# Performance work log

Measured on AMD Instinct MI355X. Metric: run time of the kernel, lower is better.

The kernel has to match this reference:

```python
import jax, jax.numpy as jnp
import numpy as np

T, B, I, H, L = 256, 128, 512, 1024, 4

def setup_inputs() -> dict:
    key = jax.random.key(0)
    ks = jax.random.split(key, 8)
    s = 1.0 / np.sqrt(H)  # ~PyTorch GRU init scale U(-1/sqrt(H), 1/sqrt(H))
    x = jax.random.normal(ks[0], (T, B, I), dtype=jnp.float32)
    hidden = jnp.zeros((L, B, H), dtype=jnp.float32)  # initHidden
    w_ih0 = jax.random.normal(ks[1], (3 * H, I), dtype=jnp.float32) * s
    w_ih_rest = jax.random.normal(ks[2], (L - 1, 3 * H, H), dtype=jnp.float32) * s
    w_hh = jax.random.normal(ks[3], (L, 3 * H, H), dtype=jnp.float32) * s
    b_ih = jax.random.normal(ks[4], (L, 3 * H), dtype=jnp.float32) * s
    b_hh = jax.random.normal(ks[5], (L, 3 * H), dtype=jnp.float32) * s
    input_lengths = jax.random.randint(ks[6], (B,), 1, T + 1)
    return {"x": x, "hidden": hidden, "w_ih0": w_ih0, "w_ih_rest": w_ih_rest,
            "w_hh": w_hh, "b_ih": b_ih, "b_hh": b_hh,
            "total_length": T, "input_lengths": input_lengths}

def _gru_layer(xs, h0, w_ih, w_hh_l, bi, bh, mask):
    # xs: (T,B,D_in); h0: (B,H); mask: (T,B) bool (t < length)
    gi = jnp.einsum('tbd,gd->tbg', xs, w_ih) + bi  # (T,B,3H) input GEMM hoisted out of scan
    def step(h, inp):
        gi_t, m = inp  # (B,3H), (B,)
        gh = h @ w_hh_l.T + bh  # (B,3H)
        ir, iz, inn = jnp.split(gi_t, 3, axis=-1)  # PyTorch gate order: r, z, n
        hr, hz, hn = jnp.split(gh, 3, axis=-1)
        r = jax.nn.sigmoid(ir + hr)
        z = jax.nn.sigmoid(iz + hz)
        n = jnp.tanh(inn + r * hn)
        h_new = (1.0 - z) * n + z * h
        m2 = m[:, None]
        h_next = jnp.where(m2, h_new, h)            # packed-seq: state frozen past length
        y = jnp.where(m2, h_new, jnp.zeros_like(h))  # pad_packed_sequence zero-pads output
        return h_next, y
    hT, ys = jax.lax.scan(step, h0, (gi, mask))
    return ys, hT

def reference(x, hidden, w_ih0, w_ih_rest, w_hh, b_ih, b_hh, total_length, input_lengths):
    # dropout=0.2 between layers is disabled (deterministic / eval mode)
    mask = jnp.arange(total_length)[:, None] < input_lengths[None, :]  # (T,B)
    ys = x
    h_finals = []
    for l in range(L):
        w_ih_l = w_ih0 if l == 0 else w_ih_rest[l - 1]
        ys, hT = _gru_layer(ys, hidden[l], w_ih_l, w_hh[l], b_ih[l], b_hh[l], mask)
        h_finals.append(hT)
    return ys, jnp.stack(h_finals, axis=0)  # (T,B,H), (4,B,H)
```

## Files before the change

kernel.cpp:

```cpp
#include <hip/hip_runtime.h>
#include <hip/hip_bf16.h>

#define T_STEPS 256
#define BATCH   128
#define IDIM    512
#define HDIM    1024
#define NLAYERS 4
#define G3      (3 * HDIM)
#define BH      (BATCH * HDIM)

typedef __bf16 bf16_t;
typedef __bf16 bf16x4 __attribute__((ext_vector_type(4)));
typedef __bf16 bf16x8 __attribute__((ext_vector_type(8)));
typedef float  f32x4  __attribute__((ext_vector_type(4)));

__device__ __forceinline__ float sigm_f(float x) { return 1.0f / (1.0f + __expf(-x)); }
__device__ __forceinline__ float tanh_f(float x) { return 1.0f - 2.0f / (__expf(2.0f * x) + 1.0f); }

__device__ __forceinline__ bf16x8 cvt8(const float* p) {
    f32x4 v0 = *(const f32x4*)p;
    f32x4 v1 = *(const f32x4*)(p + 4);
    bf16x8 o;
    o[0] = (bf16_t)v0[0]; o[1] = (bf16_t)v0[1]; o[2] = (bf16_t)v0[2]; o[3] = (bf16_t)v0[3];
    o[4] = (bf16_t)v1[0]; o[5] = (bf16_t)v1[1]; o[6] = (bf16_t)v1[2]; o[7] = (bf16_t)v1[3];
    return o;
}

__global__ void cvt_f2b(const float* __restrict__ s, bf16_t* __restrict__ d, int n4) {
    int i = blockIdx.x * blockDim.x + threadIdx.x;
    if (i < n4) {
        f32x4 v = ((const f32x4*)s)[i];
        bf16x4 o;
        o[0] = (bf16_t)v[0]; o[1] = (bf16_t)v[1];
        o[2] = (bf16_t)v[2]; o[3] = (bf16_t)v[3];
        ((bf16x4*)d)[i] = o;
    }
}

__global__ void split_h(const float* __restrict__ s,
                        bf16_t* __restrict__ hi, bf16_t* __restrict__ lo) {
    int i = blockIdx.x * blockDim.x + threadIdx.x;
    f32x4 v = ((const f32x4*)s)[i];
    bf16x4 h, l;
#pragma unroll
    for (int j = 0; j < 4; ++j) {
        bf16_t t = (bf16_t)v[j];
        h[j] = t;
        l[j] = (bf16_t)(v[j] - (float)t);
    }
    ((bf16x4*)hi)[i] = h;
    ((bf16x4*)lo)[i] = l;
}

template <int HIN>
__global__ __launch_bounds__(64)
void gi_gemm(const float*  __restrict__ ysrc,
             const bf16_t* __restrict__ w_ih,
             const float*  __restrict__ b_ih,
             float* __restrict__ gi,
             int row0)
{
    const int lane = threadIdx.x;
    const int cq   = lane & 15;
    const int quad = lane >> 4;
    const int n0   = blockIdx.x * 64;
    const int m0   = blockIdx.y * 32;

    const float* a0p = ysrc + (size_t)(row0 + m0 + cq) * HIN + quad * 8;
    const float* a1p = a0p + (size_t)16 * HIN;
    const bf16_t* b0p = w_ih + (size_t)(n0 + cq) * HIN + quad * 8;
    const bf16_t* b1p = b0p + (size_t)16 * HIN;
    const bf16_t* b2p = b0p + (size_t)32 * HIN;
    const bf16_t* b3p = b0p + (size_t)48 * HIN;

    f32x4 a00{0,0,0,0}, a01 = a00, a02 = a00, a03 = a00;
    f32x4 a10 = a00, a11 = a00, a12 = a00, a13 = a00;

#pragma unroll 4
    for (int k = 0; k < HIN; k += 32) {
        bf16x8 fa0 = cvt8(a0p + k);
        bf16x8 fa1 = cvt8(a1p + k);
        bf16x8 fb0 = *(const bf16x8*)(b0p + k);
        bf16x8 fb1 = *(const bf16x8*)(b1p + k);
        bf16x8 fb2 = *(const bf16x8*)(b2p + k);
        bf16x8 fb3 = *(const bf16x8*)(b3p + k);
        a00 = __builtin_amdgcn_mfma_f32_16x16x32_bf16(fa0, fb0, a00, 0, 0, 0);
        a01 = __builtin_amdgcn_mfma_f32_16x16x32_bf16(fa0, fb1, a01, 0, 0, 0);
        a02 = __builtin_amdgcn_mfma_f32_16x16x32_bf16(fa0, fb2, a02, 0, 0, 0);
        a03 = __builtin_amdgcn_mfma_f32_16x16x32_bf16(fa0, fb3, a03, 0, 0, 0);
        a10 = __builtin_amdgcn_mfma_f32_16x16x32_bf16(fa1, fb0, a10, 0, 0, 0);
        a11 = __builtin_amdgcn_mfma_f32_16x16x32_bf16(fa1, fb1, a11, 0, 0, 0);
        a12 = __builtin_amdgcn_mfma_f32_16x16x32_bf16(fa1, fb2, a12, 0, 0, 0);
        a13 = __builtin_amdgcn_mfma_f32_16x16x32_bf16(fa1, fb3, a13, 0, 0, 0);
    }

    const float bb0 = b_ih[n0 + 0  + cq];
    const float bb1 = b_ih[n0 + 16 + cq];
    const float bb2 = b_ih[n0 + 32 + cq];
    const float bb3 = b_ih[n0 + 48 + cq];

#pragma unroll
    for (int i = 0; i < 4; ++i) {
        const int r0 = m0 + quad * 4 + i;
        const int r1 = r0 + 16;
        float* g0 = gi + (size_t)r0 * G3 + n0 + cq;
        float* g1 = gi + (size_t)r1 * G3 + n0 + cq;
        g0[0]  = a00[i] + bb0;  g0[16] = a01[i] + bb1;
        g0[32] = a02[i] + bb2;  g0[48] = a03[i] + bb3;
        g1[0]  = a10[i] + bb0;  g1[16] = a11[i] + bb1;
        g1[32] = a12[i] + bb2;  g1[48] = a13[i] + bb3;
    }
}

struct LayerStep {
    const float*  gi_t;
    const bf16_t* w_hh;
    const float*  b_hh;
    const bf16_t* h_in_hi;
    const bf16_t* h_in_lo;
    bf16_t*       h_out_hi;
    bf16_t*       h_out_lo;
    float*        y_t;
    float*        h_final;
    int           t;
};
struct StepArgs { LayerStep L[NLAYERS]; };

__global__ __launch_bounds__(512)
void gru_step_multi(StepArgs args, const int* __restrict__ lengths)
{
    __shared__ f32x4 red[4][3][2][2][2][64];

    const LayerStep& A = args.L[blockIdx.z];

    const int tid  = threadIdx.x;
    const int wid  = tid >> 6;
    const int lane = tid & 63;
    const int cq   = lane & 15;
    const int quad = lane >> 4;
    const int c0   = blockIdx.x * 32;
    const int m0   = blockIdx.y * 64;

    const int kq = wid & 3;
    const int rh = wid >> 2;
    const int kofs = kq * 256 + quad * 8;

    const bf16_t* aph0 = A.h_in_hi + (size_t)(m0 + rh * 32 + cq) * HDIM + kofs;
    const bf16_t* aph1 = aph0 + (size_t)16 * HDIM;
    const bf16_t* apl0 = A.h_in_lo + (size_t)(m0 + rh * 32 + cq) * HDIM + kofs;
    const bf16_t* apl1 = apl0 + (size_t)16 * HDIM;
    const bf16_t* bp00 = A.w_hh + (size_t)(0 * HDIM + c0 + cq) * HDIM + kofs;
    const bf16_t* bp01 = bp00 + (size_t)16 * HDIM;
    const bf16_t* bp10 = A.w_hh + (size_t)(1 * HDIM + c0 + cq) * HDIM + kofs;
    const bf16_t* bp11 = bp10 + (size_t)16 * HDIM;
    const bf16_t* bp20 = A.w_hh + (size_t)(2 * HDIM + c0 + cq) * HDIM + kofs;
    const bf16_t* bp21 = bp20 + (size_t)16 * HDIM;

    f32x4 acc[2][2][3];
#pragma unroll
    for (int rf = 0; rf < 2; ++rf)
#pragma unroll
        for (int cf = 0; cf < 2; ++cf)
#pragma unroll
            for (int g = 0; g < 3; ++g) acc[rf][cf][g] = f32x4{0, 0, 0, 0};

#pragma unroll
    for (int k = 0; k < 256; k += 32) {
        bf16x8 Ah[2], Al[2], Bv[3][2];
        Ah[0] = *(const bf16x8*)(aph0 + k);
        Ah[1] = *(const bf16x8*)(aph1 + k);
        Al[0] = *(const bf16x8*)(apl0 + k);
        Al[1] = *(const bf16x8*)(apl1 + k);
        Bv[0][0] = *(const bf16x8*)(bp00 + k);
        Bv[0][1] = *(const bf16x8*)(bp01 + k);
        Bv[1][0] = *(const bf16x8*)(bp10 + k);
        Bv[1][1] = *(const bf16x8*)(bp11 + k);
        Bv[2][0] = *(const bf16x8*)(bp20 + k);
        Bv[2][1] = *(const bf16x8*)(bp21 + k);
#pragma unroll
        for (int rf = 0; rf < 2; ++rf)
#pragma unroll
            for (int cf = 0; cf < 2; ++cf)
#pragma unroll
                for (int g = 0; g < 3; ++g)
                    acc[rf][cf][g] = __builtin_amdgcn_mfma_f32_16x16x32_bf16(
                        Ah[rf], Bv[g][cf], acc[rf][cf][g], 0, 0, 0);
#pragma unroll
        for (int rf = 0; rf < 2; ++rf)
#pragma unroll
            for (int cf = 0; cf < 2; ++cf)
#pragma unroll
                for (int g = 0; g < 3; ++g)
                    acc[rf][cf][g] = __builtin_amdgcn_mfma_f32_16x16x32_bf16(
                        Al[rf], Bv[g][cf], acc[rf][cf][g], 0, 0, 0);
    }

#pragma unroll
    for (int rf = 0; rf < 2; ++rf)
#pragma unroll
        for (int cf = 0; cf < 2; ++cf)
#pragma unroll
            for (int g = 0; g < 3; ++g)
                red[kq][g][rh][rf][cf][lane] = acc[rf][cf][g];
    __syncthreads();

    {
        const int grh = wid & 1;
        const int grf = (wid >> 1) & 1;
        const int gcf = wid >> 2;
        const int col = c0 + gcf * 16 + cq;

        f32x4 sr = ((red[0][0][grh][grf][gcf][lane] + red[1][0][grh][grf][gcf][lane])
                  +  red[2][0][grh][grf][gcf][lane]) + red[3][0][grh][grf][gcf][lane];
        f32x4 sz = ((red[0][1][grh][grf][gcf][lane] + red[1][1][grh][grf][gcf][lane])
                  +  red[2][1][grh][grf][gcf][lane]) + red[3][1][grh][grf][gcf][lane];
        f32x4 sn = ((red[0][2][grh][grf][gcf][lane] + red[1][2][grh][grf][gcf][lane])
                  +  red[2][2][grh][grf][gcf][lane]) + red[3][2][grh][grf][gcf][lane];

        const float bhr = A.b_hh[col];
        const float bhz = A.b_hh[HDIM + col];
        const float bhn = A.b_hh[2 * HDIM + col];

#pragma unroll
        for (int i = 0; i < 4; ++i) {
            const int row = m0 + grh * 32 + grf * 16 + quad * 4 + i;
            const size_t oh = (size_t)row * HDIM + col;
            const float* gr = A.gi_t + (size_t)row * G3;
            const float ir  = gr[col];
            const float iz  = gr[HDIM + col];
            const float inn = gr[2 * HDIM + col];
            const float hold = (float)A.h_in_hi[oh] + (float)A.h_in_lo[oh];
            const float r = sigm_f(ir + sr[i] + bhr);
            const float z = sigm_f(iz + sz[i] + bhz);
            const float n = tanh_f(inn + r * (sn[i] + bhn));
            const float hnew = (1.0f - z) * n + z * hold;
            const bool msk = A.t < lengths[row];
            const float hnext = msk ? hnew : hold;
            const bf16_t hb = (bf16_t)hnext;
            A.h_out_hi[oh] = hb;
            A.h_out_lo[oh] = (bf16_t)(hnext - (float)hb);
            A.y_t[oh] = msk ? hnew : 0.0f;
            if (A.h_final) A.h_final[oh] = hnext;
        }
    }
}

extern "C" void kernel_launch(void* const* d_in, const int* in_sizes, int n_in,
                              void* d_out, int out_size, void* d_ws, size_t ws_size,
                              hipStream_t stream) {
    const float* x         = (const float*)d_in[0];
    const float* hidden    = (const float*)d_in[1];
    const float* w_ih0     = (const float*)d_in[2];
    const float* w_ih_rest = (const float*)d_in[3];
    const float* w_hh      = (const float*)d_in[4];
    const float* b_ih      = (const float*)d_in[5];
    const float* b_hh      = (const float*)d_in[6];
    const int*   lengths   = (const int*)d_in[8];

    float* ys   = (float*)d_out;
    float* hfin = ys + (size_t)T_STEPS * BH;

    char* ws = (char*)d_ws;
    bf16_t* wb_ih0  = (bf16_t*)ws;
    bf16_t* wb_rest = wb_ih0 + (size_t)G3 * IDIM;
    bf16_t* wb_hh   = wb_rest + (size_t)(NLAYERS - 1) * G3 * HDIM;
    bf16_t* hbase   = wb_hh + (size_t)NLAYERS * G3 * HDIM;
    float*  gi_base = (float*)(hbase + (size_t)NLAYERS * 4 * BH);

    const size_t fixed_bytes = (size_t)((char*)gi_base - ws);
    int chunk = 16;
    while (chunk > 2 &&
           fixed_bytes + (size_t)NLAYERS * chunk * BATCH * G3 * sizeof(float) > ws_size)
        chunk >>= 1;
    const int nch = T_STEPS / chunk;
    const size_t gi_stride = (size_t)chunk * BATCH * G3;

    {
        int n4;
        n4 = G3 * IDIM / 4;
        cvt_f2b<<<(n4 + 255) / 256, 256, 0, stream>>>(w_ih0, wb_ih0, n4);
        n4 = (NLAYERS - 1) * G3 * HDIM / 4;
        cvt_f2b<<<(n4 + 255) / 256, 256, 0, stream>>>(w_ih_rest, wb_rest, n4);
        n4 = NLAYERS * G3 * HDIM / 4;
        cvt_f2b<<<(n4 + 255) / 256, 256, 0, stream>>>(w_hh, wb_hh, n4);
    }

    for (int l = 0; l < NLAYERS; ++l) {
        bf16_t* hb = hbase + (size_t)l * 4 * BH;
        split_h<<<BH / 4 / 256, 256, 0, stream>>>(hidden + (size_t)l * BH, hb, hb + BH);
    }

    const dim3 gridA(G3 / 64, chunk * BATCH / 32);

    for (int s = 0; s < nch + NLAYERS - 1; ++s) {
        for (int l = 0; l < NLAYERS; ++l) {
            const int c = s - l;
            if (c < 0 || c >= nch) continue;
            float* gi_l = gi_base + (size_t)l * gi_stride;
            const bf16_t* wb_ih_l = (l == 0) ? wb_ih0 : (wb_rest + (size_t)(l - 1) * G3 * HDIM);
            const float*  b_ih_l  = b_ih + (size_t)l * G3;
            const int row0 = c * chunk * BATCH;
            if (l == 0) {
                gi_gemm<IDIM><<<gridA, 64, 0, stream>>>(x, wb_ih_l, b_ih_l, gi_l, row0);
            } else {
                gi_gemm<HDIM><<<gridA, 64, 0, stream>>>(ys, wb_ih_l, b_ih_l, gi_l, row0);
            }
        }
        for (int tt = 0; tt < chunk; ++tt) {
            StepArgs sa;
            int na = 0;
            for (int l = 0; l < NLAYERS; ++l) {
                const int c = s - l;
                if (c < 0 || c >= nch) continue;
                const int t = c * chunk + tt;
                const bool rd0 = ((t & 1) == 0);
                bf16_t* hb = hbase + (size_t)l * 4 * BH;
                bf16_t* hhi0 = hb, *hlo0 = hb + BH, *hhi1 = hb + 2 * BH, *hlo1 = hb + 3 * BH;
                LayerStep& P = sa.L[na++];
                P.gi_t     = gi_base + (size_t)l * gi_stride + (size_t)tt * BATCH * G3;
                P.w_hh     = wb_hh + (size_t)l * G3 * HDIM;
                P.b_hh     = b_hh + (size_t)l * G3;
                P.h_in_hi  = rd0 ? hhi0 : hhi1;
                P.h_in_lo  = rd0 ? hlo0 : hlo1;
                P.h_out_hi = rd0 ? hhi1 : hhi0;
                P.h_out_lo = rd0 ? hlo1 : hlo0;
                P.y_t      = ys + (size_t)t * BH;
                P.h_final  = (t == T_STEPS - 1) ? (hfin + (size_t)l * BH) : nullptr;
                P.t        = t;
            }
            dim3 gridB(HDIM / 32, BATCH / 64, na);
            gru_step_multi<<<gridB, 512, 0, stream>>>(sa, lengths);
        }
    }
}
```

Baseline: 12.14 ms.

## Fuse input-gate GEMM into per-step GRU kernel with bf16 ring buffers

Removes the separate chunked gi_gemm launches and computes the input projection inside the recurrent step kernel, accumulating r/z gates from both input and hidden contributions in shared accumulators. Inter-layer activations are kept as bf16 in a per-layer ring buffer, and x is pre-converted to bf16, so the fp32 gi scratch traffic and kernel launches disappear. The trade-off is more MFMA work and weight bandwidth on the serial critical path of every step, since the input GEMM no longer runs as a large batched GEMM. The ring of 2*CHUNK slots relies on the wavefront layer schedule to avoid overwriting activations that have not yet been consumed.

```diff
diff --git a/kernel.cpp b/kernel.cpp
--- a/kernel.cpp
+++ b/kernel.cpp
@@ -8,6 +8,8 @@
 #define NLAYERS 4
 #define G3      (3 * HDIM)
 #define BH      (BATCH * HDIM)
+#define CHUNK   16
+#define RING    (2 * CHUNK)
 
 typedef __bf16 bf16_t;
 typedef __bf16 bf16x4 __attribute__((ext_vector_type(4)));
@@ -16,15 +18,6 @@
 
 __device__ __forceinline__ float sigm_f(float x) { return 1.0f / (1.0f + __expf(-x)); }
 __device__ __forceinline__ float tanh_f(float x) { return 1.0f - 2.0f / (__expf(2.0f * x) + 1.0f); }
-
-__device__ __forceinline__ bf16x8 cvt8(const float* p) {
-    f32x4 v0 = *(const f32x4*)p;
-    f32x4 v1 = *(const f32x4*)(p + 4);
-    bf16x8 o;
-    o[0] = (bf16_t)v0[0]; o[1] = (bf16_t)v0[1]; o[2] = (bf16_t)v0[2]; o[3] = (bf16_t)v0[3];
-    o[4] = (bf16_t)v1[0]; o[5] = (bf16_t)v1[1]; o[6] = (bf16_t)v1[2]; o[7] = (bf16_t)v1[3];
-    return o;
-}
 
 __global__ void cvt_f2b(const float* __restrict__ s, bf16_t* __restrict__ d, int n4) {
     int i = blockIdx.x * blockDim.x + threadIdx.x;
@@ -52,84 +45,28 @@
     ((bf16x4*)lo)[i] = l;
 }
 
-template <int HIN>
-__global__ __launch_bounds__(64)
-void gi_gemm(const float*  __restrict__ ysrc,
-             const bf16_t* __restrict__ w_ih,
-             const float*  __restrict__ b_ih,
-             float* __restrict__ gi,
-             int row0)
-{
-    const int lane = threadIdx.x;
-    const int cq   = lane & 15;
-    const int quad = lane >> 4;
-    const int n0   = blockIdx.x * 64;
-    const int m0   = blockIdx.y * 32;
-
-    const float* a0p = ysrc + (size_t)(row0 + m0 + cq) * HIN + quad * 8;
-    const float* a1p = a0p + (size_t)16 * HIN;
-    const bf16_t* b0p = w_ih + (size_t)(n0 + cq) * HIN + quad * 8;
-    const bf16_t* b1p = b0p + (size_t)16 * HIN;
-    const bf16_t* b2p = b0p + (size_t)32 * HIN;
-    const bf16_t* b3p = b0p + (size_t)48 * HIN;
-
-    f32x4 a00{0,0,0,0}, a01 = a00, a02 = a00, a03 = a00;
-    f32x4 a10 = a00, a11 = a00, a12 = a00, a13 = a00;
-
-#pragma unroll 4
-    for (int k = 0; k < HIN; k += 32) {
-        bf16x8 fa0 = cvt8(a0p + k);
-        bf16x8 fa1 = cvt8(a1p + k);
-        bf16x8 fb0 = *(const bf16x8*)(b0p + k);
-        bf16x8 fb1 = *(const bf16x8*)(b1p + k);
-        bf16x8 fb2 = *(const bf16x8*)(b2p + k);
-        bf16x8 fb3 = *(const bf16x8*)(b3p + k);
-        a00 = __builtin_amdgcn_mfma_f32_16x16x32_bf16(fa0, fb0, a00, 0, 0, 0);
-        a01 = __builtin_amdgcn_mfma_f32_16x16x32_bf16(fa0, fb1, a01, 0, 0, 0);
-        a02 = __builtin_amdgcn_mfma_f32_16x16x32_bf16(fa0, fb2, a02, 0, 0, 0);
-        a03 = __builtin_amdgcn_mfma_f32_16x16x32_bf16(fa0, fb3, a03, 0, 0, 0);
-        a10 = __builtin_amdgcn_mfma_f32_16x16x32_bf16(fa1, fb0, a10, 0, 0, 0);
-        a11 = __builtin_amdgcn_mfma_f32_16x16x32_bf16(fa1, fb1, a11, 0, 0, 0);
-        a12 = __builtin_amdgcn_mfma_f32_16x16x32_bf16(fa1, fb2, a12, 0, 0, 0);
-        a13 = __builtin_amdgcn_mfma_f32_16x16x32_bf16(fa1, fb3, a13, 0, 0, 0);
-    }
-
-    const float bb0 = b_ih[n0 + 0  + cq];
-    const float bb1 = b_ih[n0 + 16 + cq];
-    const float bb2 = b_ih[n0 + 32 + cq];
-    const float bb3 = b_ih[n0 + 48 + cq];
-
-#pragma unroll
-    for (int i = 0; i < 4; ++i) {
-        const int r0 = m0 + quad * 4 + i;
-        const int r1 = r0 + 16;
-        float* g0 = gi + (size_t)r0 * G3 + n0 + cq;
-        float* g1 = gi + (size_t)r1 * G3 + n0 + cq;
-        g0[0]  = a00[i] + bb0;  g0[16] = a01[i] + bb1;
-        g0[32] = a02[i] + bb2;  g0[48] = a03[i] + bb3;
-        g1[0]  = a10[i] + bb0;  g1[16] = a11[i] + bb1;
-        g1[32] = a12[i] + bb2;  g1[48] = a13[i] + bb3;
-    }
-}
-
 struct LayerStep {
-    const float*  gi_t;
+    const bf16_t* inp;
+    const bf16_t* w_ih;
     const bf16_t* w_hh;
+    const float*  b_ih;
     const float*  b_hh;
     const bf16_t* h_in_hi;
     const bf16_t* h_in_lo;
     bf16_t*       h_out_hi;
     bf16_t*       h_out_lo;
-    float*        y_t;
+    bf16_t*       y_bf;
+    float*        y_f32;
     float*        h_final;
     int           t;
+    int           kin;
 };
 struct StepArgs { LayerStep L[NLAYERS]; };
 
 __global__ __launch_bounds__(512)
 void gru_step_multi(StepArgs args, const int* __restrict__ lengths)
 {
-    __shared__ f32x4 red[4][3][2][2][2][64];
+    __shared__ f32x4 red[4][4][2][2][2][64];
 
     const LayerStep& A = args.L[blockIdx.z];
 
@@ -143,65 +80,118 @@
 
     const int kq = wid & 3;
     const int rh = wid >> 2;
-    const int kofs = kq * 256 + quad * 8;
-
-    const bf16_t* aph0 = A.h_in_hi + (size_t)(m0 + rh * 32 + cq) * HDIM + kofs;
-    const bf16_t* aph1 = aph0 + (size_t)16 * HDIM;
-    const bf16_t* apl0 = A.h_in_lo + (size_t)(m0 + rh * 32 + cq) * HDIM + kofs;
-    const bf16_t* apl1 = apl0 + (size_t)16 * HDIM;
-    const bf16_t* bp00 = A.w_hh + (size_t)(0 * HDIM + c0 + cq) * HDIM + kofs;
-    const bf16_t* bp01 = bp00 + (size_t)16 * HDIM;
-    const bf16_t* bp10 = A.w_hh + (size_t)(1 * HDIM + c0 + cq) * HDIM + kofs;
-    const bf16_t* bp11 = bp10 + (size_t)16 * HDIM;
-    const bf16_t* bp20 = A.w_hh + (size_t)(2 * HDIM + c0 + cq) * HDIM + kofs;
-    const bf16_t* bp21 = bp20 + (size_t)16 * HDIM;
-
-    f32x4 acc[2][2][3];
+
+    f32x4 arz[2][2][2];
+    f32x4 ahn[2][2];
+    f32x4 ain[2][2];
 #pragma unroll
     for (int rf = 0; rf < 2; ++rf)
 #pragma unroll
-        for (int cf = 0; cf < 2; ++cf)
-#pragma unroll
-            for (int g = 0; g < 3; ++g) acc[rf][cf][g] = f32x4{0, 0, 0, 0};
-
-#pragma unroll
-    for (int k = 0; k < 256; k += 32) {
-        bf16x8 Ah[2], Al[2], Bv[3][2];
-        Ah[0] = *(const bf16x8*)(aph0 + k);
-        Ah[1] = *(const bf16x8*)(aph1 + k);
-        Al[0] = *(const bf16x8*)(apl0 + k);
-        Al[1] = *(const bf16x8*)(apl1 + k);
-        Bv[0][0] = *(const bf16x8*)(bp00 + k);
-        Bv[0][1] = *(const bf16x8*)(bp01 + k);
-        Bv[1][0] = *(const bf16x8*)(bp10 + k);
-        Bv[1][1] = *(const bf16x8*)(bp11 + k);
-        Bv[2][0] = *(const bf16x8*)(bp20 + k);
-        Bv[2][1] = *(const bf16x8*)(bp21 + k);
-#pragma unroll
-        for (int rf = 0; rf < 2; ++rf)
-#pragma unroll
-            for (int cf = 0; cf < 2; ++cf)
-#pragma unroll
-                for (int g = 0; g < 3; ++g)
-                    acc[rf][cf][g] = __builtin_amdgcn_mfma_f32_16x16x32_bf16(
-                        Ah[rf], Bv[g][cf], acc[rf][cf][g], 0, 0, 0);
-#pragma unroll
-        for (int rf = 0; rf < 2; ++rf)
-#pragma unroll
-            for (int cf = 0; cf < 2; ++cf)
-#pragma unroll
-                for (int g = 0; g < 3; ++g)
-                    acc[rf][cf][g] = __builtin_amdgcn_mfma_f32_16x16x32_bf16(
-                        Al[rf], Bv[g][cf], acc[rf][cf][g], 0, 0, 0);
+        for (int cf = 0; cf < 2; ++cf) {
+            arz[rf][cf][0] = f32x4{0, 0, 0, 0};
+            arz[rf][cf][1] = f32x4{0, 0, 0, 0};
+            ahn[rf][cf]    = f32x4{0, 0, 0, 0};
+            ain[rf][cf]    = f32x4{0, 0, 0, 0};
+        }
+
+    {
+        const int kofs = kq * 256 + quad * 8;
+        const bf16_t* aph0 = A.h_in_hi + (size_t)(m0 + rh * 32 + cq) * HDIM + kofs;
+        const bf16_t* aph1 = aph0 + (size_t)16 * HDIM;
+        const bf16_t* apl0 = A.h_in_lo + (size_t)(m0 + rh * 32 + cq) * HDIM + kofs;
+        const bf16_t* apl1 = apl0 + (size_t)16 * HDIM;
+        const bf16_t* bp00 = A.w_hh + (size_t)(0 * HDIM + c0 + cq) * HDIM + kofs;
+        const bf16_t* bp01 = bp00 + (size_t)16 * HDIM;
+        const bf16_t* bp10 = A.w_hh + (size_t)(1 * HDIM + c0 + cq) * HDIM + kofs;
+        const bf16_t* bp11 = bp10 + (size_t)16 * HDIM;
+        const bf16_t* bp20 = A.w_hh + (size_t)(2 * HDIM + c0 + cq) * HDIM + kofs;
+        const bf16_t* bp21 = bp20 + (size_t)16 * HDIM;
+
+#pragma unroll
+        for (int k = 0; k < 256; k += 32) {
+            bf16x8 Ah[2], Al[2], Bv[3][2];
+            Ah[0] = *(const bf16x8*)(aph0 + k);
+            Ah[1] = *(const bf16x8*)(aph1 + k);
+            Al[0] = *(const bf16x8*)(apl0 + k);
+            Al[1] = *(const bf16x8*)(apl1 + k);
+            Bv[0][0] = *(const bf16x8*)(bp00 + k);
+            Bv[0][1] = *(const bf16x8*)(bp01 + k);
+            Bv[1][0] = *(const bf16x8*)(bp10 + k);
+            Bv[1][1] = *(const bf16x8*)(bp11 + k);
+            Bv[2][0] = *(const bf16x8*)(bp20 + k);
+            Bv[2][1] = *(const bf16x8*)(bp21 + k);
+#pragma unroll
+            for (int rf = 0; rf < 2; ++rf)
+#pragma unroll
+                for (int cf = 0; cf < 2; ++cf) {
+                    arz[rf][cf][0] = __builtin_amdgcn_mfma_f32_16x16x32_bf16(
+                        Ah[rf], Bv[0][cf], arz[rf][cf][0], 0, 0, 0);
+                    arz[rf][cf][1] = __builtin_amdgcn_mfma_f32_16x16x32_bf16(
+                        Ah[rf], Bv[1][cf], arz[rf][cf][1], 0, 0, 0);
+                    ahn[rf][cf] = __builtin_amdgcn_mfma_f32_16x16x32_bf16(
+                        Ah[rf], Bv[2][cf], ahn[rf][cf], 0, 0, 0);
+                }
+#pragma unroll
+            for (int rf = 0; rf < 2; ++rf)
+#pragma unroll
+                for (int cf = 0; cf < 2; ++cf) {
+                    arz[rf][cf][0] = __builtin_amdgcn_mfma_f32_16x16x32_bf16(
+                        Al[rf], Bv[0][cf], arz[rf][cf][0], 0, 0, 0);
+                    arz[rf][cf][1] = __builtin_amdgcn_mfma_f32_16x16x32_bf16(
+                        Al[rf], Bv[1][cf], arz[rf][cf][1], 0, 0, 0);
+                    ahn[rf][cf] = __builtin_amdgcn_mfma_f32_16x16x32_bf16(
+                        Al[rf], Bv[2][cf], ahn[rf][cf], 0, 0, 0);
+                }
+        }
+    }
+
+    {
+        const int kin  = A.kin;
+        const int qw   = kin >> 2;
+        const int kofs = kq * qw + quad * 8;
+        const bf16_t* axp0 = A.inp + (size_t)(m0 + rh * 32 + cq) * kin + kofs;
+        const bf16_t* axp1 = axp0 + (size_t)16 * kin;
+        const bf16_t* wp00 = A.w_ih + (size_t)(0 * HDIM + c0 + cq) * kin + kofs;
+        const bf16_t* wp01 = wp00 + (size_t)16 * kin;
+        const bf16_t* wp10 = A.w_ih + (size_t)(1 * HDIM + c0 + cq) * kin + kofs;
+        const bf16_t* wp11 = wp10 + (size_t)16 * kin;
+        const bf16_t* wp20 = A.w_ih + (size_t)(2 * HDIM + c0 + cq) * kin + kofs;
+        const bf16_t* wp21 = wp20 + (size_t)16 * kin;
+
+#pragma unroll 4
+        for (int k = 0; k < qw; k += 32) {
+            bf16x8 Ax[2], Wv[3][2];
+            Ax[0] = *(const bf16x8*)(axp0 + k);
+            Ax[1] = *(const bf16x8*)(axp1 + k);
+            Wv[0][0] = *(const bf16x8*)(wp00 + k);
+            Wv[0][1] = *(const bf16x8*)(wp01 + k);
+            Wv[1][0] = *(const bf16x8*)(wp10 + k);
+            Wv[1][1] = *(const bf16x8*)(wp11 + k);
+            Wv[2][0] = *(const bf16x8*)(wp20 + k);
+            Wv[2][1] = *(const bf16x8*)(wp21 + k);
+#pragma unroll
+            for (int rf = 0; rf < 2; ++rf)
+#pragma unroll
+                for (int cf = 0; cf < 2; ++cf) {
+                    arz[rf][cf][0] = __builtin_amdgcn_mfma_f32_16x16x32_bf16(
+                        Ax[rf], Wv[0][cf], arz[rf][cf][0], 0, 0, 0);
+                    arz[rf][cf][1] = __builtin_amdgcn_mfma_f32_16x16x32_bf16(
+                        Ax[rf], Wv[1][cf], arz[rf][cf][1], 0, 0, 0);
+                    ain[rf][cf] = __builtin_amdgcn_mfma_f32_16x16x32_bf16(
+                        Ax[rf], Wv[2][cf], ain[rf][cf], 0, 0, 0);
+                }
+        }
     }
 
 #pragma unroll
     for (int rf = 0; rf < 2; ++rf)
 #pragma unroll
-        for (int cf = 0; cf < 2; ++cf)
-#pragma unroll
-            for (int g = 0; g < 3; ++g)
-                red[kq][g][rh][rf][cf][lane] = acc[rf][cf][g];
+        for (int cf = 0; cf < 2; ++cf) {
+            red[kq][0][rh][rf][cf][lane] = arz[rf][cf][0];
+            red[kq][1][rh][rf][cf][lane] = arz[rf][cf][1];
+            red[kq][2][rh][rf][cf][lane] = ahn[rf][cf];
+            red[kq][3][rh][rf][cf][lane] = ain[rf][cf];
+        }
     __syncthreads();
 
     {
@@ -214,9 +204,14 @@
                   +  red[2][0][grh][grf][gcf][lane]) + red[3][0][grh][grf][gcf][lane];
         f32x4 sz = ((red[0][1][grh][grf][gcf][lane] + red[1][1][grh][grf][gcf][lane])
                   +  red[2][1][grh][grf][gcf][lane]) + red[3][1][grh][grf][gcf][lane];
-        f32x4 sn = ((red[0][2][grh][grf][gcf][lane] + red[1][2][grh][grf][gcf][lane])
-                  +  red[2][2][grh][grf][gcf][lane]) + red[3][2][grh][grf][gcf][lane];
-
+        f32x4 shn = ((red[0][2][grh][grf][gcf][lane] + red[1][2][grh][grf][gcf][lane])
+                   +  red[2][2][grh][grf][gcf][lane]) + red[3][2][grh][grf][gcf][lane];
+        f32x4 sin_ = ((red[0][3][grh][grf][gcf][lane] + red[1][3][grh][grf][gcf][lane])
+                    +  red[2][3][grh][grf][gcf][lane]) + red[3][3][grh][grf][gcf][lane];
+
+        const float bir = A.b_ih[col];
+        const float biz = A.b_ih[HDIM + col];
+        const float bin = A.b_ih[2 * HDIM + col];
         const float bhr = A.b_hh[col];
         const float bhz = A.b_hh[HDIM + col];
         const float bhn = A.b_hh[2 * HDIM + col];
@@ -225,21 +220,19 @@
         for (int i = 0; i < 4; ++i) {
             const int row = m0 + grh * 32 + grf * 16 + quad * 4 + i;
             const size_t oh = (size_t)row * HDIM + col;
-            const float* gr = A.gi_t + (size_t)row * G3;
-            const float ir  = gr[col];
-            const float iz  = gr[HDIM + col];
-            const float inn = gr[2 * HDIM + col];
             const float hold = (float)A.h_in_hi[oh] + (float)A.h_in_lo[oh];
-            const float r = sigm_f(ir + sr[i] + bhr);
-            const float z = sigm_f(iz + sz[i] + bhz);
-            const float n = tanh_f(inn + r * (sn[i] + bhn));
+            const float r = sigm_f(sr[i] + bir + bhr);
+            const float z = sigm_f(sz[i] + biz + bhz);
+            const float n = tanh_f((sin_[i] + bin) + r * (shn[i] + bhn));
             const float hnew = (1.0f - z) * n + z * hold;
             const bool msk = A.t < lengths[row];
             const float hnext = msk ? hnew : hold;
             const bf16_t hb = (bf16_t)hnext;
             A.h_out_hi[oh] = hb;
             A.h_out_lo[oh] = (bf16_t)(hnext - (float)hb);
-            A.y_t[oh] = msk ? hnew : 0.0f;
+            const float yv = msk ? hnew : 0.0f;
+            if (A.y_bf)  A.y_bf[oh]  = (bf16_t)yv;
+            if (A.y_f32) A.y_f32[oh] = yv;
             if (A.h_final) A.h_final[oh] = hnext;
         }
     }
@@ -265,15 +258,8 @@
     bf16_t* wb_rest = wb_ih0 + (size_t)G3 * IDIM;
     bf16_t* wb_hh   = wb_rest + (size_t)(NLAYERS - 1) * G3 * HDIM;
     bf16_t* hbase   = wb_hh + (size_t)NLAYERS * G3 * HDIM;
-    float*  gi_base = (float*)(hbase + (size_t)NLAYERS * 4 * BH);
-
-    const size_t fixed_bytes = (size_t)((char*)gi_base - ws);
-    int chunk = 16;
-    while (chunk > 2 &&
-           fixed_bytes + (size_t)NLAYERS * chunk * BATCH * G3 * sizeof(float) > ws_size)
-        chunk >>= 1;
-    const int nch = T_STEPS / chunk;
-    const size_t gi_stride = (size_t)chunk * BATCH * G3;
+    bf16_t* xb      = hbase + (size_t)NLAYERS * 4 * BH;
+    bf16_t* ybuf    = xb + (size_t)T_STEPS * BATCH * IDIM;
 
     {
         int n4;
@@ -283,6 +269,8 @@
         cvt_f2b<<<(n4 + 255) / 256, 256, 0, stream>>>(w_ih_rest, wb_rest, n4);
         n4 = NLAYERS * G3 * HDIM / 4;
         cvt_f2b<<<(n4 + 255) / 256, 256, 0, stream>>>(w_hh, wb_hh, n4);
+        n4 = T_STEPS * BATCH * IDIM / 4;
+        cvt_f2b<<<(n4 + 255) / 256, 256, 0, stream>>>(x, xb, n4);
     }
 
     for (int l = 0; l < NLAYERS; ++l) {
@@ -290,41 +278,41 @@
         split_h<<<BH / 4 / 256, 256, 0, stream>>>(hidden + (size_t)l * BH, hb, hb + BH);
     }
 
-    const dim3 gridA(G3 / 64, chunk * BATCH / 32);
+    const int nch = T_STEPS / CHUNK;
 
     for (int s = 0; s < nch + NLAYERS - 1; ++s) {
-        for (int l = 0; l < NLAYERS; ++l) {
-            const int c = s - l;
-            if (c < 0 || c >= nch) continue;
-            float* gi_l = gi_base + (size_t)l * gi_stride;
-            const bf16_t* wb_ih_l = (l == 0) ? wb_ih0 : (wb_rest + (size_t)(l - 1) * G3 * HDIM);
-            const float*  b_ih_l  = b_ih + (size_t)l * G3;
-            const int row0 = c * chunk * BATCH;
-            if (l == 0) {
-                gi_gemm<IDIM><<<gridA, 64, 0, stream>>>(x, wb_ih_l, b_ih_l, gi_l, row0);
-            } else {
-                gi_gemm<HDIM><<<gridA, 64, 0, stream>>>(ys, wb_ih_l, b_ih_l, gi_l, row0);
-            }
-        }
-        for (int tt = 0; tt < chunk; ++tt) {
+        for (int tt = 0; tt < CHUNK; ++tt) {
             StepArgs sa;
             int na = 0;
             for (int l = 0; l < NLAYERS; ++l) {
                 const int c = s - l;
                 if (c < 0 || c >= nch) continue;
-                const int t = c * chunk + tt;
+                const int t = c * CHUNK + tt;
                 const bool rd0 = ((t & 1) == 0);
                 bf16_t* hb = hbase + (size_t)l * 4 * BH;
                 bf16_t* hhi0 = hb, *hlo0 = hb + BH, *hhi1 = hb + 2 * BH, *hlo1 = hb + 3 * BH;
                 LayerStep& P = sa.L[na++];
-                P.gi_t     = gi_base + (size_t)l * gi_stride + (size_t)tt * BATCH * G3;
+                if (l == 0) {
+                    P.inp = xb + (size_t)t * BATCH * IDIM;
+                    P.kin = IDIM;
+                    P.w_ih = wb_ih0;
+                } else {
+                    P.inp = ybuf + (size_t)(l - 1) * RING * BH
+                                 + (size_t)(t & (RING - 1)) * BH;
+                    P.kin = HDIM;
+                    P.w_ih = wb_rest + (size_t)(l - 1) * G3 * HDIM;
+                }
                 P.w_hh     = wb_hh + (size_t)l * G3 * HDIM;
+                P.b_ih     = b_ih + (size_t)l * G3;
                 P.b_hh     = b_hh + (size_t)l * G3;
                 P.h_in_hi  = rd0 ? hhi0 : hhi1;
                 P.h_in_lo  = rd0 ? hlo0 : hlo1;
                 P.h_out_hi = rd0 ? hhi1 : hhi0;
                 P.h_out_lo = rd0 ? hlo1 : hlo0;
-                P.y_t      = ys + (size_t)t * BH;
+                P.y_bf     = (l < NLAYERS - 1)
+                           ? (ybuf + (size_t)l * RING * BH + (size_t)(t & (RING - 1)) * BH)
+                           : nullptr;
+                P.y_f32    = (l == NLAYERS - 1) ? (ys + (size_t)t * BH) : nullptr;
                 P.h_final  = (t == T_STEPS - 1) ? (hfin + (size_t)l * BH) : nullptr;
                 P.t        = t;
             }
```

Result: faster. 11.14 ms (-8.2%).
